# Kernel tuning notes

Measured on AMD Instinct MI355X. Metric: run time of the kernel, lower is better.

Reference implementation:

```python
import jax, jax.numpy as jnp
import numpy as np

N_NODES = 100000
N_EDGES = 1600000
N_GRAPHS = 4096
EPS = 1e-5


def setup_inputs() -> dict:
    key = jax.random.key(0)
    ks = jax.random.split(key, 12)
    x = jax.random.normal(ks[0], (N_NODES, 9), dtype=jnp.float32)
    edge_index = jax.random.randint(ks[1], (2, N_EDGES), 0, N_NODES, dtype=jnp.int64)
    batch = jnp.sort(jax.random.randint(ks[2], (N_NODES,), 0, N_GRAPHS, dtype=jnp.int64))
    w0 = jax.random.normal(ks[3], (9, 128), dtype=jnp.float32) * 0.3
    w12 = jax.random.normal(ks[4], (2, 128, 128), dtype=jnp.float32) * 0.09
    cb = jax.random.normal(ks[5], (3, 128), dtype=jnp.float32) * 0.02
    bn_g = jnp.ones((3, 128), dtype=jnp.float32)
    bn_b = jnp.zeros((3, 128), dtype=jnp.float32)
    m0w = jax.random.normal(ks[6], (256, 256), dtype=jnp.float32) * 0.06
    m0b = jnp.zeros((256,), dtype=jnp.float32)
    m1w = jax.random.normal(ks[7], (256, 64), dtype=jnp.float32) * 0.06
    m1b = jnp.zeros((64,), dtype=jnp.float32)
    m2w = jax.random.normal(ks[8], (64, 1), dtype=jnp.float32) * 0.12
    m2b = jnp.zeros((1,), dtype=jnp.float32)
    return {"x": x, "edge_index": edge_index, "batch": batch, "w0": w0, "w12": w12,
            "cb": cb, "bn_g": bn_g, "bn_b": bn_b, "m0w": m0w, "m0b": m0b,
            "m1w": m1w, "m1b": m1b, "m2w": m2w, "m2b": m2b}


def reference(x, edge_index, batch, w0, w12, cb, bn_g, bn_b, m0w, m0b, m1w, m1b, m2w, m2b):
    N = x.shape[0]
    loops = jnp.arange(N, dtype=edge_index.dtype)
    src = jnp.concatenate([edge_index[0], loops])  # [E+N]
    dst = jnp.concatenate([edge_index[1], loops])
    # symmetric GCN normalization with self-loops: deg^-1/2 on both ends
    deg = jax.ops.segment_sum(jnp.ones(src.shape, dtype=x.dtype), dst, num_segments=N)
    dinv = jax.lax.rsqrt(jnp.maximum(deg, 1.0))
    enorm = (dinv[src] * dinv[dst])[:, None]  # [E+N, 1]

    def gcn_bn_relu(h, W, b, g, beta):
        h = h @ W                                            # [N, H]
        agg = jax.ops.segment_sum(h[src] * enorm, dst, num_segments=N) + b
        mu = agg.mean(axis=0)
        var = agg.var(axis=0)  # biased, as in BatchNorm training forward
        hn = (agg - mu) * jax.lax.rsqrt(var + EPS) * g + beta
        return jax.nn.relu(hn)

    h = gcn_bn_relu(x, w0, cb[0], bn_g[0], bn_b[0])
    h = gcn_bn_relu(h, w12[0], cb[1], bn_g[1], bn_b[1])
    h = gcn_bn_relu(h, w12[1], cb[2], bn_g[2], bn_b[2])

    # global mean / max pool over graphs
    cnt = jax.ops.segment_sum(jnp.ones((N,), dtype=h.dtype), batch, num_segments=N_GRAPHS)
    xs = jax.ops.segment_sum(h, batch, num_segments=N_GRAPHS)
    x_mean = xs / jnp.maximum(cnt, 1.0)[:, None]
    x_max = jax.ops.segment_max(h, batch, num_segments=N_GRAPHS)
    x_max = jnp.where(jnp.isfinite(x_max), x_max, 0.0)
    xg = jnp.concatenate([x_mean, x_max], axis=1)  # [G, 256]

    hm = jax.nn.relu(xg @ m0w + m0b)
    hm = jax.nn.relu(hm @ m1w + m1b)
    out = hm @ m2w + m2b
    return out[:, 0]
```

## Files before the change

kernel.cpp:

```cpp
#include <hip/hip_runtime.h>

#define NN 100000
#define NE 1600000
#define NG 4096
#define HD 128
#define EPSV 1e-5f
#define NBUCK 391
#define BIN_CHUNK 4096
#define NBIN_BLK ((NE + BIN_CHUNK - 1) / BIN_CHUNK)
#define CSR_CAP 8448
#define NB_AG 4096
#define CH_AG 25
#define NB_MM 2048
#define CH_MM 49

typedef _Float16 half_t;
typedef _Float16 half8 __attribute__((ext_vector_type(8)));
typedef _Float16 half4v __attribute__((ext_vector_type(4)));
typedef _Float16 half2v __attribute__((ext_vector_type(2)));
typedef float f32x4 __attribute__((ext_vector_type(4)));


__global__ void k_zero_i32(int* p, int n) {
    int i = blockIdx.x * blockDim.x + threadIdx.x;
    if (i < n) p[i] = 0;
}

__global__ void k_bcount(const int* __restrict__ ei, int* __restrict__ bcnt) {
    __shared__ int cnt[NBUCK];
    int t = threadIdx.x;
    for (int i = t; i < NBUCK; i += 256) cnt[i] = 0;
    __syncthreads();
    int e0 = blockIdx.x * BIN_CHUNK;
    int e1 = min(NE, e0 + BIN_CHUNK);
    for (int e = e0 + t; e < e1; e += 256)
        atomicAdd(&cnt[ei[NE + e] >> 8], 1);
    __syncthreads();
    for (int i = t; i < NBUCK; i += 256)
        if (cnt[i]) atomicAdd(&bcnt[i], cnt[i]);
}

__global__ void k_bscan(const int* __restrict__ bcnt, int* __restrict__ ebase, int* __restrict__ gcur) {
    __shared__ int s[512];
    int t = threadIdx.x;
    int v = (t < NBUCK) ? bcnt[t] : 0;
    s[t] = v;
    __syncthreads();
    for (int off = 1; off < 512; off <<= 1) {
        int x = (t >= off) ? s[t - off] : 0;
        __syncthreads();
        s[t] += x;
        __syncthreads();
    }
    if (t <= NBUCK) {
        int ex = s[t] - v;
        ebase[t] = ex;
        if (t < NBUCK) gcur[t] = ex;
    }
}

__global__ void k_bin(const int* __restrict__ ei, int* __restrict__ gcur, unsigned* __restrict__ binned) {
    __shared__ int cnt[NBUCK];
    __shared__ int cur[NBUCK];
    int t = threadIdx.x;
    for (int i = t; i < NBUCK; i += 256) cnt[i] = 0;
    __syncthreads();
    int e0 = blockIdx.x * BIN_CHUNK;
    int e1 = min(NE, e0 + BIN_CHUNK);
    for (int e = e0 + t; e < e1; e += 256)
        atomicAdd(&cnt[ei[NE + e] >> 8], 1);
    __syncthreads();
    for (int i = t; i < NBUCK; i += 256)
        cur[i] = cnt[i] ? atomicAdd(&gcur[i], cnt[i]) : 0;
    __syncthreads();
    for (int e = e0 + t; e < e1; e += 256) {
        int d = ei[NE + e];
        int b = d >> 8;
        int r = atomicAdd(&cur[b], 1);
        binned[r] = ((unsigned)ei[e] << 8) | (unsigned)(d & 255);
    }
}

__global__ __launch_bounds__(256) void k_csr(const unsigned* __restrict__ binned,
        const int* __restrict__ ebase, int* __restrict__ rp,
        float* __restrict__ dinv, int* __restrict__ col) {
    __shared__ int colb[CSR_CAP];
    __shared__ int deg[256], cur[256], s[256];
    int b = blockIdx.x, t = threadIdx.x;
    int n0 = b * 256;
    int nodes = min(256, NN - n0);
    int cbeg = ebase[b];
    int cnt_b = min(ebase[b + 1] - cbeg, CSR_CAP - 256);
    int base = cbeg + n0;
    deg[t] = 0;
    __syncthreads();
    for (int i = t; i < cnt_b; i += 256)
        atomicAdd(&deg[binned[cbeg + i] & 255], 1);
    __syncthreads();
    int w = (t < nodes) ? deg[t] + 1 : 0;
    s[t] = w;
    __syncthreads();
    for (int o = 1; o < 256; o <<= 1) {
        int x = (t >= o) ? s[t - o] : 0;
        __syncthreads();
        s[t] += x;
        __syncthreads();
    }
    int ex = s[t] - w;
    cur[t] = ex;
    if (t < nodes) {
        rp[n0 + t] = base + ex;
        dinv[n0 + t] = rsqrtf((float)(deg[t] + 1));
    }
    __syncthreads();
    for (int i = t; i < cnt_b; i += 256) {
        unsigned pk = binned[cbeg + i];
        int d = pk & 255;
        int r = atomicAdd(&cur[d], 1);
        colb[r] = (int)(pk >> 8);
    }
    __syncthreads();
    if (t < nodes) colb[cur[t]] = n0 + t;
    __syncthreads();
    int tot = cnt_b + nodes;
    for (int i = t; i < tot; i += 256) col[base + i] = colb[i];
    if (b == 0 && t == 0) rp[NN] = NE + NN;
}


__global__ void k_prep(const float* __restrict__ w12, half_t* __restrict__ Wt,
                       const float* __restrict__ x, const float* __restrict__ dinv,
                       half_t* __restrict__ xh, const int* __restrict__ batch,
                       int* __restrict__ gstart) {
    int b = blockIdx.x;
    if (b < 16) {
        int g = b * 256 + threadIdx.x;
        int lo = 0, hi = NN;
        while (lo < hi) { int m = (lo + hi) >> 1; if (batch[m] < g) lo = m + 1; else hi = m; }
        gstart[g] = lo;
        if (g == 0) gstart[NG] = NN;
    } else if (b < 144) {
        int i = (b - 16) * 256 + threadIdx.x;
        int m = i >> 14;
        int r = i & 16383;
        int n = r >> 7, k = r & 127;
        Wt[i] = (half_t)w12[m * 16384 + k * 128 + n];
    } else {
        int n = (b - 144) * 256 + threadIdx.x;
        if (n >= NN) return;
        float dv = dinv[n];
        half_t buf[16];
#pragma unroll
        for (int k = 0; k < 9; ++k) buf[k] = (half_t)(x[n * 9 + k] * dv);
#pragma unroll
        for (int k = 9; k < 16; ++k) buf[k] = (half_t)0.f;
        *(half8*)&xh[n * 16] = *(half8*)buf;
        *(half8*)&xh[n * 16 + 8] = *(half8*)(buf + 8);
    }
}


__global__ void k_aggx(const half_t* __restrict__ xh, const float* __restrict__ dinv,
                       half_t* __restrict__ aggx,
                       const int* __restrict__ rp, const int* __restrict__ col) {
    int t = blockIdx.x * blockDim.x + threadIdx.x;
    int n = t >> 2, sub = (t & 3) * 4;
    if (n >= NN) return;
    int s = rp[n], e = rp[n + 1];
    float acc[4] = {0.f, 0.f, 0.f, 0.f};
    int i = s;
    for (; i + 1 < e; i += 2) {
        half4v v0 = *(const half4v*)&xh[col[i] * 16 + sub];
        half4v v1 = *(const half4v*)&xh[col[i + 1] * 16 + sub];
#pragma unroll
        for (int j = 0; j < 4; ++j) acc[j] += (float)v0[j] + (float)v1[j];
    }
    if (i < e) {
        half4v v0 = *(const half4v*)&xh[col[i] * 16 + sub];
#pragma unroll
        for (int j = 0; j < 4; ++j) acc[j] += (float)v0[j];
    }
    float dv = dinv[n];
    half4v o = {(half_t)(acc[0] * dv), (half_t)(acc[1] * dv),
                (half_t)(acc[2] * dv), (half_t)(acc[3] * dv)};
    *(half4v*)&aggx[n * 16 + sub] = o;
}

__global__ __launch_bounds__(256) void k_mm9(const half_t* __restrict__ aggx,
        const float* __restrict__ w0, half_t* __restrict__ gout,
        float* __restrict__ ps, float* __restrict__ ps2) {
    __shared__ float lsum[4][128], lsq[4][128];
    int t = threadIdx.x, w = t >> 6, l = t & 63;
    int c = 2 * l;
    int n0 = blockIdx.x * CH_MM;
    int n1 = min(NN, n0 + CH_MM);
    float s0 = 0.f, s1 = 0.f, q0 = 0.f, q1 = 0.f;
    for (int n = n0 + w; n < n1; n += 4) {
        float2 acc = make_float2(0.f, 0.f);
#pragma unroll
        for (int k = 0; k < 9; ++k) {
            float a = (float)aggx[n * 16 + k];
            float2 wv = *(const float2*)&w0[k * HD + c];
            acc.x += a * wv.x;
            acc.y += a * wv.y;
        }
        half_t hx = (half_t)acc.x, hy = (half_t)acc.y;
        half2v hv = {hx, hy};
        *(half2v*)&gout[n * HD + c] = hv;
        float fx = (float)hx, fy = (float)hy;
        s0 += fx; q0 += fx * fx; s1 += fy; q1 += fy * fy;
    }
    lsum[w][c] = s0; lsum[w][c + 1] = s1;
    lsq[w][c] = q0;  lsq[w][c + 1] = q1;
    __syncthreads();
    if (t < 128) {
        ps[blockIdx.x * 128 + t] = lsum[0][t] + lsum[1][t] + lsum[2][t] + lsum[3][t];
        ps2[blockIdx.x * 128 + t] = lsq[0][t] + lsq[1][t] + lsq[2][t] + lsq[3][t];
    }
}

__global__ __launch_bounds__(256) void k_stats2(const float* __restrict__ ps,
        const float* __restrict__ ps2, const float* __restrict__ g,
        const float* __restrict__ be, float* __restrict__ scale,
        float* __restrict__ shift, int nb) {
    __shared__ float sa[256], sb[256];
    int c = blockIdx.x, t = threadIdx.x;
    float S = 0.f, Q = 0.f;
    for (int i = t; i < nb; i += 256) {
        S += ps[i * 128 + c];
        Q += ps2[i * 128 + c];
    }
    sa[t] = S; sb[t] = Q;
    __syncthreads();
    for (int o = 128; o; o >>= 1) {
        if (t < o) { sa[t] += sa[t + o]; sb[t] += sb[t + o]; }
        __syncthreads();
    }
    if (t == 0) {
        double mu = (double)sa[0] / NN;
        double var = (double)sb[0] / NN - mu * mu;
        float sc = g[c] * rsqrtf((float)var + EPSV);
        scale[c] = sc;
        shift[c] = be[c] - (float)mu * sc;
    }
}


__global__ __launch_bounds__(256) void k_mm_mfma(const half_t* __restrict__ gf,
        const float* __restrict__ scale, const float* __restrict__ shift,
        const float* __restrict__ dinv, const half_t* __restrict__ Wt,
        half_t* __restrict__ hh) {
    __shared__ half_t wlds[16384];
    int t = threadIdx.x;
#pragma unroll
    for (int j = 0; j < 8; ++j) {
        int cidx = t * 8 + j;
        int n = cidx >> 4, k8 = cidx & 15;
        half8 v = *(const half8*)&Wt[cidx * 8];
        int byte = n * 256 + ((k8 * 16) ^ ((n & 7) << 4));
        *(half8*)((char*)wlds + byte) = v;
    }
    __syncthreads();
    int w = t >> 6, l = t & 63;
    int lr = l & 15, lg = l >> 4;
    int base = (blockIdx.x * 4 + w) * 16;
    int row = base + lr;
    bool rowok = row < NN;
    f32x4 acc[8];
#pragma unroll
    for (int nt = 0; nt < 8; ++nt) acc[nt] = (f32x4){0.f, 0.f, 0.f, 0.f};
#pragma unroll
    for (int kk = 0; kk < 4; ++kk) {
        int ch0 = kk * 32 + lg * 8;
        half8 a8;
        if (rowok) {
            half8 hv = *(const half8*)&gf[row * HD + ch0];
            f32x4 sc0 = *(const f32x4*)&scale[ch0];
            f32x4 sc1 = *(const f32x4*)&scale[ch0 + 4];
            f32x4 sh0 = *(const f32x4*)&shift[ch0];
            f32x4 sh1 = *(const f32x4*)&shift[ch0 + 4];
#pragma unroll
            for (int i = 0; i < 4; ++i)
                a8[i] = (half_t)fmaxf((float)hv[i] * sc0[i] + sh0[i], 0.f);
#pragma unroll
            for (int i = 0; i < 4; ++i)
                a8[4 + i] = (half_t)fmaxf((float)hv[4 + i] * sc1[i] + sh1[i], 0.f);
        } else {
#pragma unroll
            for (int i = 0; i < 8; ++i) a8[i] = (half_t)0.f;
        }
        int kbyte = kk * 64 + lg * 16;
#pragma unroll
        for (int nt = 0; nt < 8; ++nt) {
            int n = nt * 16 + lr;
            half8 b8 = *(const half8*)((const char*)wlds + n * 256 + (kbyte ^ ((n & 7) << 4)));
            acc[nt] = __builtin_amdgcn_mfma_f32_16x16x32_f16(a8, b8, acc[nt], 0, 0, 0);
        }
    }
#pragma unroll
    for (int i = 0; i < 4; ++i) {
        int r = base + lg * 4 + i;
        if (r < NN) {
            float dv = dinv[r];
#pragma unroll
            for (int nt = 0; nt < 8; ++nt)
                hh[r * HD + nt * 16 + lr] = (half_t)(acc[nt][i] * dv);
        }
    }
}


__global__ __launch_bounds__(256) void k_agg_h(const half_t* __restrict__ hh,
        const float* __restrict__ dinv, half_t* __restrict__ gout,
        const int* __restrict__ rp, const int* __restrict__ col,
        float* __restrict__ ps, float* __restrict__ ps2) {
    __shared__ float lsum[16][128], lsq[16][128];
    int t = threadIdx.x, w = t >> 6, l = t & 63;
    int sub = l >> 4, li = l & 15;
    int sg = w * 4 + sub;
    int c0 = li * 8;
    int n0 = blockIdx.x * CH_AG;
    int n1 = min(NN, n0 + CH_AG);
    float sacc[8], qacc[8];
#pragma unroll
    for (int j = 0; j < 8; ++j) { sacc[j] = 0.f; qacc[j] = 0.f; }
    for (int n = n0 + sg; n < n1; n += 16) {
        int s = rp[n], e = rp[n + 1];
        float facc[8];
#pragma unroll
        for (int j = 0; j < 8; ++j) facc[j] = 0.f;
        int i = s;
        for (; i + 1 < e; i += 2) {
            int ca = col[i], cb = col[i + 1];
            half8 v0 = *(const half8*)&hh[ca * HD + c0];
            half8 v1 = *(const half8*)&hh[cb * HD + c0];
#pragma unroll
            for (int j = 0; j < 8; ++j) facc[j] += (float)v0[j] + (float)v1[j];
        }
        if (i < e) {
            half8 v0 = *(const half8*)&hh[col[i] * HD + c0];
#pragma unroll
            for (int j = 0; j < 8; ++j) facc[j] += (float)v0[j];
        }
        float dv = dinv[n];
        half8 hv;
#pragma unroll
        for (int j = 0; j < 8; ++j) hv[j] = (half_t)(facc[j] * dv);
        *(half8*)&gout[n * HD + c0] = hv;
#pragma unroll
        for (int j = 0; j < 8; ++j) {
            float f = (float)hv[j];
            sacc[j] += f;
            qacc[j] += f * f;
        }
    }
#pragma unroll
    for (int j = 0; j < 8; ++j) {
        lsum[sg][c0 + j] = sacc[j];
        lsq[sg][c0 + j] = qacc[j];
    }
    __syncthreads();
    if (t < 128) {
        float S = 0.f, Q = 0.f;
#pragma unroll
        for (int g = 0; g < 16; ++g) { S += lsum[g][t]; Q += lsq[g][t]; }
        ps[blockIdx.x * 128 + t] = S;
        ps2[blockIdx.x * 128 + t] = Q;
    }
}


__global__ void k_pool(const half_t* __restrict__ h, const float* __restrict__ scale,
                       const float* __restrict__ shift, const int* __restrict__ gstart,
                       float* __restrict__ xg) {
    int l = threadIdx.x & 63;
    int g = blockIdx.x * (blockDim.x >> 6) + (threadIdx.x >> 6);
    if (g >= NG) return;
    int c = 2 * l;
    float2 sc = make_float2(scale[c], scale[c + 1]);
    float2 sh = make_float2(shift[c], shift[c + 1]);
    int s = gstart[g], e = gstart[g + 1];
    float2 sum = make_float2(0.f, 0.f), mx = make_float2(-3e38f, -3e38f);
    for (int r = s; r < e; ++r) {
        half2v hv = *(const half2v*)&h[r * HD + c];
        float vx = fmaxf((float)hv[0] * sc.x + sh.x, 0.f);
        float vy = fmaxf((float)hv[1] * sc.y + sh.y, 0.f);
        sum.x += vx; sum.y += vy;
        mx.x = fmaxf(mx.x, vx); mx.y = fmaxf(mx.y, vy);
    }
    float2 mean = make_float2(0.f, 0.f), mxo = make_float2(0.f, 0.f);
    if (e > s) {
        float cnt = (float)(e - s);
        mean.x = sum.x / cnt; mean.y = sum.y / cnt;
        mxo = mx;
    }
    *(float2*)&xg[g * 256 + c] = mean;
    *(float2*)&xg[g * 256 + 128 + c] = mxo;
}

#define GPB 8
__global__ __launch_bounds__(256) void k_mlp(const float* __restrict__ xg,
                                             const float* __restrict__ m0w, const float* __restrict__ m0b,
                                             const float* __restrict__ m1w, const float* __restrict__ m1b,
                                             const float* __restrict__ m2w, const float* __restrict__ m2b,
                                             float* __restrict__ out) {
    __shared__ float xs[GPB][256];
    __shared__ float h1[GPB][256];
    __shared__ float h2[GPB][64];
    int t = threadIdx.x;
    int g0 = blockIdx.x * GPB;
#pragma unroll
    for (int j = 0; j < GPB; ++j) xs[j][t] = xg[(g0 + j) * 256 + t];
    __syncthreads();
    float acc[GPB];
#pragma unroll
    for (int j = 0; j < GPB; ++j) acc[j] = m0b[t];
    for (int i = 0; i < 256; ++i) {
        float wv = m0w[i * 256 + t];
#pragma unroll
        for (int j = 0; j < GPB; ++j) acc[j] += xs[j][i] * wv;
    }
#pragma unroll
    for (int j = 0; j < GPB; ++j) h1[j][t] = fmaxf(acc[j], 0.f);
    __syncthreads();
    if (t < 64) {
        float a2[GPB];
#pragma unroll
        for (int j = 0; j < GPB; ++j) a2[j] = m1b[t];
        for (int i = 0; i < 256; ++i) {
            float wv = m1w[i * 64 + t];
#pragma unroll
            for (int j = 0; j < GPB; ++j) a2[j] += h1[j][i] * wv;
        }
#pragma unroll
        for (int j = 0; j < GPB; ++j) h2[j][t] = fmaxf(a2[j], 0.f);
    }
    __syncthreads();
    if (t < 64) {
#pragma unroll
        for (int j = 0; j < GPB; ++j) {
            float v = h2[j][t] * m2w[t];
            for (int off = 32; off; off >>= 1) v += __shfl_down(v, off);
            if (t == 0) out[g0 + j] = v + m2b[0];
        }
    }
}


extern "C" void kernel_launch(void* const* d_in, const int* in_sizes, int n_in,
                              void* d_out, int out_size, void* d_ws, size_t ws_size,
                              hipStream_t stream) {
    const float* x    = (const float*)d_in[0];
    const int*   ei   = (const int*)d_in[1];
    const int*   batch= (const int*)d_in[2];
    const float* w0   = (const float*)d_in[3];
    const float* w12  = (const float*)d_in[4];
    const float* bn_g = (const float*)d_in[6];
    const float* bn_b = (const float*)d_in[7];
    const float* m0w  = (const float*)d_in[8];
    const float* m0b  = (const float*)d_in[9];
    const float* m1w  = (const float*)d_in[10];
    const float* m1b  = (const float*)d_in[11];
    const float* m2w  = (const float*)d_in[12];
    const float* m2b  = (const float*)d_in[13];
    float* out = (float*)d_out;

    char* p = (char*)d_ws;
    auto alloc = [&](size_t bytes) {
        void* r = (void*)p;
        p += (bytes + 255) & ~(size_t)255;
        return r;
    };
    half_t*   gf0    = (half_t*)alloc((size_t)NN * HD * 2);
    half_t*   gf1    = (half_t*)alloc((size_t)NN * HD * 2);
    half_t*   hh     = (half_t*)alloc((size_t)NN * HD * 2);
    half_t*   xh     = (half_t*)alloc((size_t)NN * 16 * 2);
    half_t*   aggx   = (half_t*)alloc((size_t)NN * 16 * 2);
    half_t*   Wt     = (half_t*)alloc((size_t)2 * 128 * 128 * 2);
    float*    dinv   = (float*)alloc((size_t)NN * 4);
    int*      rp     = (int*)alloc((size_t)(NN + 1) * 4);
    int*      col    = (int*)alloc((size_t)(NE + NN) * 4);
    unsigned* binned = (unsigned*)alloc((size_t)NE * 4);
    int*      bcnt   = (int*)alloc(512 * 4);
    int*      ebase  = (int*)alloc(512 * 4);
    int*      gcur   = (int*)alloc(512 * 4);
    int*      gstart = (int*)alloc((size_t)(NG + 1) * 4);
    float*    ps     = (float*)alloc((size_t)NB_AG * 128 * 4);
    float*    ps2    = (float*)alloc((size_t)NB_AG * 128 * 4);
    float*    scb    = (float*)alloc(3 * 128 * 4);
    float*    shb    = (float*)alloc(3 * 128 * 4);
    float*    xg     = (float*)alloc((size_t)NG * 256 * 4);

    k_zero_i32<<<2, 256, 0, stream>>>(bcnt, 512);
    k_bcount<<<NBIN_BLK, 256, 0, stream>>>(ei, bcnt);
    k_bscan<<<1, 512, 0, stream>>>(bcnt, ebase, gcur);
    k_bin<<<NBIN_BLK, 256, 0, stream>>>(ei, gcur, binned);
    k_csr<<<NBUCK, 256, 0, stream>>>(binned, ebase, rp, dinv, col);

    k_prep<<<144 + (NN + 255) / 256, 256, 0, stream>>>(w12, Wt, x, dinv, xh, batch, gstart);

    k_aggx<<<(NN * 4 + 255) / 256, 256, 0, stream>>>(xh, dinv, aggx, rp, col);
    k_mm9<<<NB_MM, 256, 0, stream>>>(aggx, w0, gf0, ps, ps2);
    k_stats2<<<128, 256, 0, stream>>>(ps, ps2, bn_g + 0, bn_b + 0, scb + 0, shb + 0, NB_MM);

    k_mm_mfma<<<(NN + 63) / 64, 256, 0, stream>>>(gf0, scb + 0, shb + 0, dinv, Wt, hh);
    k_agg_h<<<NB_AG, 256, 0, stream>>>(hh, dinv, gf1, rp, col, ps, ps2);
    k_stats2<<<128, 256, 0, stream>>>(ps, ps2, bn_g + 128, bn_b + 128, scb + 128, shb + 128, NB_AG);

    k_mm_mfma<<<(NN + 63) / 64, 256, 0, stream>>>(gf1, scb + 128, shb + 128, dinv, Wt + 16384, hh);
    k_agg_h<<<NB_AG, 256, 0, stream>>>(hh, dinv, gf0, rp, col, ps, ps2);
    k_stats2<<<128, 256, 0, stream>>>(ps, ps2, bn_g + 256, bn_b + 256, scb + 256, shb + 256, NB_AG);

    k_pool<<<NG / 4, 256, 0, stream>>>(gf0, scb + 256, shb + 256, gstart, xg);
    k_mlp<<<NG / GPB, 256, 0, stream>>>(xg, m0w, m0b, m1w, m1b, m2w, m2b, out);
}
```

Before: 361.1 us.

## Fuse layer-0 aggregation with 9-wide matmul and split pooling across two waves

Merges the layer-0 neighbour aggregation and the 9x128 projection into one kernel. The aggregated features for 64 nodes stay in shared memory and the weights are held in registers, which removes the aggx intermediate buffer and one kernel launch. Separately, global pooling now uses two wavefronts per graph, each covering half the rows, and combines them through shared memory to double parallelism on that pass. The cost is an extra block-wide sync and some idle half-wavefronts in each kernel.

```diff
diff --git a/kernel.cpp b/kernel.cpp
--- a/kernel.cpp
+++ b/kernel.cpp
@@ -11,8 +11,7 @@
 #define CSR_CAP 8448
 #define NB_AG 4096
 #define CH_AG 25
-#define NB_MM 2048
-#define CH_MM 49
+#define NB_L0 1563
 
 typedef _Float16 half_t;
 typedef _Float16 half8 __attribute__((ext_vector_type(8)));
@@ -160,49 +159,56 @@
 }
 
 
-__global__ void k_aggx(const half_t* __restrict__ xh, const float* __restrict__ dinv,
-                       half_t* __restrict__ aggx,
-                       const int* __restrict__ rp, const int* __restrict__ col) {
-    int t = blockIdx.x * blockDim.x + threadIdx.x;
-    int n = t >> 2, sub = (t & 3) * 4;
-    if (n >= NN) return;
-    int s = rp[n], e = rp[n + 1];
-    float acc[4] = {0.f, 0.f, 0.f, 0.f};
-    int i = s;
-    for (; i + 1 < e; i += 2) {
-        half4v v0 = *(const half4v*)&xh[col[i] * 16 + sub];
-        half4v v1 = *(const half4v*)&xh[col[i + 1] * 16 + sub];
-#pragma unroll
-        for (int j = 0; j < 4; ++j) acc[j] += (float)v0[j] + (float)v1[j];
-    }
-    if (i < e) {
-        half4v v0 = *(const half4v*)&xh[col[i] * 16 + sub];
-#pragma unroll
-        for (int j = 0; j < 4; ++j) acc[j] += (float)v0[j];
-    }
-    float dv = dinv[n];
-    half4v o = {(half_t)(acc[0] * dv), (half_t)(acc[1] * dv),
-                (half_t)(acc[2] * dv), (half_t)(acc[3] * dv)};
-    *(half4v*)&aggx[n * 16 + sub] = o;
-}
-
-__global__ __launch_bounds__(256) void k_mm9(const half_t* __restrict__ aggx,
-        const float* __restrict__ w0, half_t* __restrict__ gout,
-        float* __restrict__ ps, float* __restrict__ ps2) {
+__global__ __launch_bounds__(256) void k_l0(const half_t* __restrict__ xh,
+        const float* __restrict__ dinv, const float* __restrict__ w0,
+        const int* __restrict__ rp, const int* __restrict__ col,
+        half_t* __restrict__ gout, float* __restrict__ ps, float* __restrict__ ps2) {
+    __shared__ float ax[64][17];
     __shared__ float lsum[4][128], lsq[4][128];
-    int t = threadIdx.x, w = t >> 6, l = t & 63;
-    int c = 2 * l;
-    int n0 = blockIdx.x * CH_MM;
-    int n1 = min(NN, n0 + CH_MM);
+    int t = threadIdx.x;
+    int n0 = blockIdx.x * 64;
+    {
+        int ln = t >> 2, sub = (t & 3) * 4;
+        int n = n0 + ln;
+        float acc[4] = {0.f, 0.f, 0.f, 0.f};
+        if (n < NN) {
+            int s = rp[n], e = rp[n + 1];
+            int i = s;
+            for (; i + 1 < e; i += 2) {
+                half4v v0 = *(const half4v*)&xh[col[i] * 16 + sub];
+                half4v v1 = *(const half4v*)&xh[col[i + 1] * 16 + sub];
+#pragma unroll
+                for (int j = 0; j < 4; ++j) acc[j] += (float)v0[j] + (float)v1[j];
+            }
+            if (i < e) {
+                half4v v0 = *(const half4v*)&xh[col[i] * 16 + sub];
+#pragma unroll
+                for (int j = 0; j < 4; ++j) acc[j] += (float)v0[j];
+            }
+            float dv = dinv[n];
+#pragma unroll
+            for (int j = 0; j < 4; ++j) ax[ln][sub + j] = acc[j] * dv;
+        } else {
+#pragma unroll
+            for (int j = 0; j < 4; ++j) ax[ln][sub + j] = 0.f;
+        }
+    }
+    __syncthreads();
+    int w = t >> 6, l = t & 63, c = 2 * l;
+    float2 wv[9];
+#pragma unroll
+    for (int k = 0; k < 9; ++k) wv[k] = *(const float2*)&w0[k * HD + c];
     float s0 = 0.f, s1 = 0.f, q0 = 0.f, q1 = 0.f;
-    for (int n = n0 + w; n < n1; n += 4) {
+    for (int j = 0; j < 16; ++j) {
+        int ln2 = w * 16 + j;
+        int n = n0 + ln2;
+        if (n >= NN) break;
         float2 acc = make_float2(0.f, 0.f);
 #pragma unroll
         for (int k = 0; k < 9; ++k) {
-            float a = (float)aggx[n * 16 + k];
-            float2 wv = *(const float2*)&w0[k * HD + c];
-            acc.x += a * wv.x;
-            acc.y += a * wv.y;
+            float a = ax[ln2][k];
+            acc.x += a * wv[k].x;
+            acc.y += a * wv[k].y;
         }
         half_t hx = (half_t)acc.x, hy = (half_t)acc.y;
         half2v hv = {hx, hy};
@@ -370,32 +376,45 @@
 }
 
 
-__global__ void k_pool(const half_t* __restrict__ h, const float* __restrict__ scale,
-                       const float* __restrict__ shift, const int* __restrict__ gstart,
-                       float* __restrict__ xg) {
-    int l = threadIdx.x & 63;
-    int g = blockIdx.x * (blockDim.x >> 6) + (threadIdx.x >> 6);
-    if (g >= NG) return;
+__global__ __launch_bounds__(256) void k_pool(const half_t* __restrict__ h,
+        const float* __restrict__ scale, const float* __restrict__ shift,
+        const int* __restrict__ gstart, float* __restrict__ xg) {
+    __shared__ float ssum[2][2][128], smax[2][2][128];
+    int t = threadIdx.x, w = t >> 6, l = t & 63;
+    int gi = w >> 1, half = w & 1;
+    int g = blockIdx.x * 2 + gi;
     int c = 2 * l;
     float2 sc = make_float2(scale[c], scale[c + 1]);
     float2 sh = make_float2(shift[c], shift[c + 1]);
     int s = gstart[g], e = gstart[g + 1];
+    int mid = (s + e) >> 1;
+    int rs = half ? mid : s;
+    int re = half ? e : mid;
     float2 sum = make_float2(0.f, 0.f), mx = make_float2(-3e38f, -3e38f);
-    for (int r = s; r < e; ++r) {
+    for (int r = rs; r < re; ++r) {
         half2v hv = *(const half2v*)&h[r * HD + c];
         float vx = fmaxf((float)hv[0] * sc.x + sh.x, 0.f);
         float vy = fmaxf((float)hv[1] * sc.y + sh.y, 0.f);
         sum.x += vx; sum.y += vy;
         mx.x = fmaxf(mx.x, vx); mx.y = fmaxf(mx.y, vy);
     }
-    float2 mean = make_float2(0.f, 0.f), mxo = make_float2(0.f, 0.f);
-    if (e > s) {
-        float cnt = (float)(e - s);
-        mean.x = sum.x / cnt; mean.y = sum.y / cnt;
-        mxo = mx;
-    }
-    *(float2*)&xg[g * 256 + c] = mean;
-    *(float2*)&xg[g * 256 + 128 + c] = mxo;
+    ssum[gi][half][c] = sum.x; ssum[gi][half][c + 1] = sum.y;
+    smax[gi][half][c] = mx.x;  smax[gi][half][c + 1] = mx.y;
+    __syncthreads();
+    if (half == 0) {
+        float2 stot = make_float2(ssum[gi][0][c] + ssum[gi][1][c],
+                                  ssum[gi][0][c + 1] + ssum[gi][1][c + 1]);
+        float2 mtot = make_float2(fmaxf(smax[gi][0][c], smax[gi][1][c]),
+                                  fmaxf(smax[gi][0][c + 1], smax[gi][1][c + 1]));
+        float2 mean = make_float2(0.f, 0.f), mxo = make_float2(0.f, 0.f);
+        if (e > s) {
+            float cnt = (float)(e - s);
+            mean.x = stot.x / cnt; mean.y = stot.y / cnt;
+            mxo = mtot;
+        }
+        *(float2*)&xg[g * 256 + c] = mean;
+        *(float2*)&xg[g * 256 + 128 + c] = mxo;
+    }
 }
 
 #define GPB 8
@@ -475,7 +494,6 @@
     half_t*   gf1    = (half_t*)alloc((size_t)NN * HD * 2);
     half_t*   hh     = (half_t*)alloc((size_t)NN * HD * 2);
     half_t*   xh     = (half_t*)alloc((size_t)NN * 16 * 2);
-    half_t*   aggx   = (half_t*)alloc((size_t)NN * 16 * 2);
     half_t*   Wt     = (half_t*)alloc((size_t)2 * 128 * 128 * 2);
     float*    dinv   = (float*)alloc((size_t)NN * 4);
     int*      rp     = (int*)alloc((size_t)(NN + 1) * 4);
@@ -499,9 +517,8 @@
 
     k_prep<<<144 + (NN + 255) / 256, 256, 0, stream>>>(w12, Wt, x, dinv, xh, batch, gstart);
 
-    k_aggx<<<(NN * 4 + 255) / 256, 256, 0, stream>>>(xh, dinv, aggx, rp, col);
-    k_mm9<<<NB_MM, 256, 0, stream>>>(aggx, w0, gf0, ps, ps2);
-    k_stats2<<<128, 256, 0, stream>>>(ps, ps2, bn_g + 0, bn_b + 0, scb + 0, shb + 0, NB_MM);
+    k_l0<<<NB_L0, 256, 0, stream>>>(xh, dinv, w0, rp, col, gf0, ps, ps2);
+    k_stats2<<<128, 256, 0, stream>>>(ps, ps2, bn_g + 0, bn_b + 0, scb + 0, shb + 0, NB_L0);
 
     k_mm_mfma<<<(NN + 63) / 64, 256, 0, stream>>>(gf0, scb + 0, shb + 0, dinv, Wt, hh);
     k_agg_h<<<NB_AG, 256, 0, stream>>>(hh, dinv, gf1, rp, col, ps, ps2);
@@ -511,6 +528,6 @@
     k_agg_h<<<NB_AG, 256, 0, stream>>>(hh, dinv, gf0, rp, col, ps, ps2);
     k_stats2<<<128, 256, 0, stream>>>(ps, ps2, bn_g + 256, bn_b + 256, scb + 256, shb + 256, NB_AG);
 
-    k_pool<<<NG / 4, 256, 0, stream>>>(gf0, scb + 256, shb + 256, gstart, xg);
+    k_pool<<<NG / 2, 256, 0, stream>>>(gf0, scb + 256, shb + 256, gstart, xg);
     k_mlp<<<NG / GPB, 256, 0, stream>>>(xg, m0w, m0b, m1w, m1b, m2w, m2b, out);
 }
```

Result: faster. 346.7 us (-4.0%).
